# Kernel tuning notes

Measured on AMD Instinct MI355X. Metric: run time of the kernel, lower is better.

The kernel has to match this reference:

```python
import jax, jax.numpy as jnp
import numpy as np

N_NODES = 20000
N_EDGES = 160000
F_IN = 256
N_CLASSES = 32
HEADS = 8
GAT_C = 128


def setup_inputs() -> dict:
    key = jax.random.key(0)
    ks = jax.random.split(key, 20)

    def w(k, shape, fan_in):
        return jax.random.normal(k, shape, dtype=jnp.float32) * (1.0 / np.sqrt(fan_in))

    return {
        "x": jax.random.normal(ks[0], (N_NODES, F_IN), dtype=jnp.float32),
        "edge_index": jax.random.randint(ks[1], (2, N_EDGES), 0, N_NODES, dtype=jnp.int64),
        # SAGEConv(256 -> 64): lin_l (bias) on aggregated neighbors, lin_r (no bias) on root
        "W_l1": w(ks[2], (F_IN, 64), F_IN), "b_l1": jnp.zeros((64,), jnp.float32),
        "W_r1": w(ks[3], (F_IN, 64), F_IN),
        # SAGEConv(64 -> 128)
        "W_l2": w(ks[4], (64, 128), 64), "b_l2": jnp.zeros((128,), jnp.float32),
        "W_r2": w(ks[5], (64, 128), 64),
        # GATConv(128 -> 128, heads=8, concat)
        "W_g": w(ks[6], (128, HEADS * GAT_C), 128),
        "att_src": w(ks[7], (HEADS, GAT_C), GAT_C),
        "att_dst": w(ks[8], (HEADS, GAT_C), GAT_C),
        "b_g": jnp.zeros((HEADS * GAT_C,), jnp.float32),
        # GCNConv(1024 -> 64), GCNConv(64 -> 32)
        "W_c1": w(ks[9], (HEADS * GAT_C, 64), HEADS * GAT_C), "b_c1": jnp.zeros((64,), jnp.float32),
        "W_c2": w(ks[10], (64, N_CLASSES), 64), "b_c2": jnp.zeros((N_CLASSES,), jnp.float32),
        # residual Linear(256 -> 64)
        "W_res": w(ks[11], (F_IN, 64), F_IN), "b_res": jnp.zeros((64,), jnp.float32),
    }


def _forward(x, edge_index, W_l1, b_l1, W_r1, W_l2, b_l2, W_r2,
             W_g, att_src, att_dst, b_g, W_c1, b_c1, W_c2, b_c2, W_res, b_res):
    n = x.shape[0]
    src, dst = edge_index[0], edge_index[1]  # messages flow src -> dst

    def sage(h, Wl, bl, Wr):
        # mean aggregation of neighbor features, then lin_l(agg) + lin_r(root)
        s = jax.ops.segment_sum(h[src], dst, num_segments=n)
        cnt = jax.ops.segment_sum(jnp.ones_like(src, dtype=h.dtype), dst, num_segments=n)
        mean = s / jnp.maximum(cnt, 1.0)[:, None]
        return mean @ Wl + bl + h @ Wr

    res_x = x @ W_res + b_res
    h = jax.nn.relu(sage(x, W_l1, b_l1, W_r1)) + res_x      # [N, 64]
    h = jax.nn.relu(sage(h, W_l2, b_l2, W_r2))              # [N, 128]

    # ---- GATConv with self-loops (PyG default) ----
    loop = jnp.arange(n, dtype=src.dtype)
    srcf = jnp.concatenate([src, loop])
    dstf = jnp.concatenate([dst, loop])

    hg = (h @ W_g).reshape(n, HEADS, GAT_C)                 # [N, H, C]
    a_s = jnp.sum(hg * att_src, axis=-1)                    # [N, H]
    a_d = jnp.sum(hg * att_dst, axis=-1)                    # [N, H]
    e = jax.nn.leaky_relu(a_s[srcf] + a_d[dstf], negative_slope=0.2)  # [Ef, H]
    m = jax.ops.segment_max(e, dstf, num_segments=n)
    e = jnp.exp(e - m[dstf])
    denom = jax.ops.segment_sum(e, dstf, num_segments=n)
    alpha = e / denom[dstf]                                 # softmax over incoming edges
    gat = jax.ops.segment_sum(alpha[:, :, None] * hg[srcf], dstf, num_segments=n)
    h = jax.nn.relu(gat.reshape(n, HEADS * GAT_C) + b_g)    # [N, 1024]

    # ---- GCNConv with self-loops and symmetric normalization ----
    deg = jax.ops.segment_sum(jnp.ones_like(srcf, dtype=h.dtype), dstf, num_segments=n)
    dinv = jax.lax.rsqrt(jnp.maximum(deg, 1.0))             # deg >= 1 via self-loops
    norm = (dinv[srcf] * dinv[dstf])[:, None]

    def gcn(h, W, b):
        hw = h @ W
        return jax.ops.segment_sum(norm * hw[srcf], dstf, num_segments=n) + b

    h = gcn(h, W_c1, b_c1)
    h = gcn(h, W_c2, b_c2)
    return jax.nn.log_softmax(h, axis=1)


def reference(x, edge_index, W_l1, b_l1, W_r1, W_l2, b_l2, W_r2,
              W_g, att_src, att_dst, b_g, W_c1, b_c1, W_c2, b_c2, W_res, b_res):
    return _forward(x, edge_index, W_l1, b_l1, W_r1, W_l2, b_l2, W_r2,
                    W_g, att_src, att_dst, b_g, W_c1, b_c1, W_c2, b_c2, W_res, b_res)
```

## Files before the change

kernel.cpp:

```cpp
#include <hip/hip_runtime.h>

#define NN 20000
#define NE 160000
#define NEF 180000
#define NB1 ((NN + 255) / 256)

typedef long long ll;
typedef __attribute__((ext_vector_type(4))) float f32x4;
typedef __attribute__((ext_vector_type(8))) short s16x8;

static __device__ __forceinline__ float b2f(ushort u) {
  return __uint_as_float(((unsigned)u) << 16);
}
static __device__ __forceinline__ ushort f2b(float f) {
  unsigned u = __float_as_uint(f);
  return (ushort)((u + 0x7fffu + ((u >> 16) & 1u)) >> 16);
}

template<int MF, int NF, int K, bool F32OUT>
__global__ __launch_bounds__(256) void gemm_mfma(
    const ushort* __restrict__ A, const ushort* __restrict__ Bt,
    const float* __restrict__ bias, void* __restrict__ Cv,
    int M, int N, int lda)
{
  const int wid  = threadIdx.x >> 6;
  const int lane = threadIdx.x & 63;
  const int wr = wid >> 1, wc = wid & 1;
  const int bm = blockIdx.y * (32 * MF) + wr * (16 * MF);
  const int bn = blockIdx.x * (32 * NF) + wc * (16 * NF);
  const int lr = lane & 15;
  const int ko = (lane >> 4) * 8;

  const ushort* pa[MF];
  const ushort* pb[NF];
  #pragma unroll
  for (int i = 0; i < MF; i++) {
    int r = min(bm + i * 16 + lr, M - 1);
    pa[i] = A + (ll)r * lda + ko;
  }
  #pragma unroll
  for (int j = 0; j < NF; j++) {
    int c = min(bn + j * 16 + lr, N - 1);
    pb[j] = Bt + (ll)c * K + ko;
  }

  f32x4 acc[MF][NF];
  #pragma unroll
  for (int i = 0; i < MF; i++)
    #pragma unroll
    for (int j = 0; j < NF; j++) acc[i][j] = {0.f, 0.f, 0.f, 0.f};

  #pragma unroll
  for (int k = 0; k < K; k += 32) {
    s16x8 af[MF], bf[NF];
    #pragma unroll
    for (int i = 0; i < MF; i++) af[i] = *(const s16x8*)(pa[i] + k);
    #pragma unroll
    for (int j = 0; j < NF; j++) bf[j] = *(const s16x8*)(pb[j] + k);
    #pragma unroll
    for (int i = 0; i < MF; i++)
      #pragma unroll
      for (int j = 0; j < NF; j++)
        acc[i][j] = __builtin_amdgcn_mfma_f32_16x16x32_bf16(af[i], bf[j], acc[i][j], 0, 0, 0);
  }

  const int rq = (lane >> 4) * 4;
  #pragma unroll
  for (int i = 0; i < MF; i++) {
    #pragma unroll
    for (int j = 0; j < NF; j++) {
      int col = bn + j * 16 + lr;
      if (col >= N) continue;
      float bv = bias ? bias[col] : 0.f;
      int rbase = bm + i * 16 + rq;
      #pragma unroll
      for (int r = 0; r < 4; r++) {
        int row = rbase + r;
        if (row >= M) continue;
        float v = acc[i][j][r] + bv;
        if (F32OUT) ((float*)Cv)[(ll)row * N + col] = v;
        else        ((ushort*)Cv)[(ll)row * N + col] = f2b(v);
      }
    }
  }
}

__global__ __launch_bounds__(256) void k_gat_apply_gcn1(
    const ushort* __restrict__ agg,
    const ushort* __restrict__ BtG,
    const ushort* __restrict__ Btc1,
    const float* __restrict__ b_g,
    ushort* __restrict__ hw64)
{
  __shared__ ushort At[2][32 * 128];
  __shared__ ushort gt[2][32][72];
  const int t    = threadIdx.x;
  const int wc   = t >> 6;
  const int lane = t & 63;
  const int bm = blockIdx.x * 32;
  const int lr = lane & 15;
  const int q  = lane >> 4;
  const int ko = q * 8;
  const int rq = q * 4;

  const int srow = t >> 3;
  const int scg  = t & 7;
  const ushort* sg = agg + (ll)min(bm + srow, NN - 1) * 1024 + scg * 16;
  const int w0 = srow * 128 + (((2 * scg)     ^ (srow & 7)) * 8);
  const int w1 = srow * 128 + (((2 * scg + 1) ^ (srow & 7)) * 8);

  s16x8 ar[8][2];
  #pragma unroll
  for (int h = 0; h < 8; h++) {
    ar[h][0] = *(const s16x8*)(sg + h * 128);
    ar[h][1] = *(const s16x8*)(sg + h * 128 + 8);
  }

  s16x8 b1[2][4];
  s16x8 b2[2][2];
  float bvs[2];
  {
    const int cg = wc * 16 + lr;
    const ushort* pb = BtG + (ll)cg * 128 + ko;
    b1[0][0] = *(const s16x8*)(pb);
    b1[0][1] = *(const s16x8*)(pb + 32);
    b1[0][2] = *(const s16x8*)(pb + 64);
    b1[0][3] = *(const s16x8*)(pb + 96);
    const ushort* qb = Btc1 + (ll)cg * 1024 + ko;
    b2[0][0] = *(const s16x8*)(qb);
    b2[0][1] = *(const s16x8*)(qb + 32);
    bvs[0] = b_g[cg];
  }

  f32x4 o0 = {0.f, 0.f, 0.f, 0.f}, o1 = o0;

  #pragma unroll
  for (int h = 0; h < 8; h++) {
    *(s16x8*)&At[h & 1][w0] = ar[h][0];
    *(s16x8*)&At[h & 1][w1] = ar[h][1];
    __syncthreads();
    #pragma unroll
    for (int it = 0; it < 2; it++) {
      const int ct = 2 * h + it;
      const int cur = it, nxt = it ^ 1;
      if (ct < 15) {
        const int cg2 = (ct + 1) * 64 + wc * 16 + lr;
        const ushort* pb2 = BtG + (ll)cg2 * 128 + ko;
        b1[nxt][0] = *(const s16x8*)(pb2);
        b1[nxt][1] = *(const s16x8*)(pb2 + 32);
        b1[nxt][2] = *(const s16x8*)(pb2 + 64);
        b1[nxt][3] = *(const s16x8*)(pb2 + 96);
        const ushort* qb2 = Btc1 + (ll)(wc * 16 + lr) * 1024 + (ct + 1) * 64 + ko;
        b2[nxt][0] = *(const s16x8*)(qb2);
        b2[nxt][1] = *(const s16x8*)(qb2 + 32);
        bvs[nxt] = b_g[cg2];
      }
      f32x4 g0 = {0.f, 0.f, 0.f, 0.f}, g1 = g0;
      #pragma unroll
      for (int k = 0; k < 4; k++) {
        const int gi = (k * 4 + q) ^ (lr & 7);
        s16x8 a0 = *(const s16x8*)&At[h & 1][lr        * 128 + gi * 8];
        s16x8 a1 = *(const s16x8*)&At[h & 1][(16 + lr) * 128 + gi * 8];
        g0 = __builtin_amdgcn_mfma_f32_16x16x32_bf16(a0, b1[cur][k], g0, 0, 0, 0);
        g1 = __builtin_amdgcn_mfma_f32_16x16x32_bf16(a1, b1[cur][k], g1, 0, 0, 0);
      }
      float bv = bvs[cur];
      #pragma unroll
      for (int r = 0; r < 4; r++) {
        gt[it][rq + r][wc * 16 + lr]      = f2b(fmaxf(g0[r] + bv, 0.f));
        gt[it][16 + rq + r][wc * 16 + lr] = f2b(fmaxf(g1[r] + bv, 0.f));
      }
      __syncthreads();
      {
        s16x8 a0 = *(const s16x8*)&gt[it][lr][ko];
        s16x8 a1 = *(const s16x8*)&gt[it][16 + lr][ko];
        o0 = __builtin_amdgcn_mfma_f32_16x16x32_bf16(a0, b2[cur][0], o0, 0, 0, 0);
        o1 = __builtin_amdgcn_mfma_f32_16x16x32_bf16(a1, b2[cur][0], o1, 0, 0, 0);
        s16x8 a2 = *(const s16x8*)&gt[it][lr][32 + ko];
        s16x8 a3 = *(const s16x8*)&gt[it][16 + lr][32 + ko];
        o0 = __builtin_amdgcn_mfma_f32_16x16x32_bf16(a2, b2[cur][1], o0, 0, 0, 0);
        o1 = __builtin_amdgcn_mfma_f32_16x16x32_bf16(a3, b2[cur][1], o1, 0, 0, 0);
      }
    }
  }
  int col = wc * 16 + lr;
  #pragma unroll
  for (int r = 0; r < 4; r++) {
    int row0 = bm + rq + r, row1 = bm + 16 + rq + r;
    if (row0 < NN) hw64[(ll)row0 * 64 + col] = f2b(o0[r]);
    if (row1 < NN) hw64[(ll)row1 * 64 + col] = f2b(o1[r]);
  }
}

struct PrepEnt { const float* W; ushort* Bt; int N; int K; int base; };
struct Prep { PrepEnt e[8]; int total; };

__global__ void k_setup(const float* __restrict__ x, ushort* __restrict__ xb, Prep p,
                        const float* __restrict__ b_res, const float* __restrict__ b_l1,
                        const float* __restrict__ b_l2, float* __restrict__ bias192,
                        float* __restrict__ bias256,
                        const float* __restrict__ W_g, const float* __restrict__ att_s,
                        const float* __restrict__ att_d, ushort* __restrict__ watt_t,
                        int* __restrict__ icnt) {
  ll t = (ll)blockIdx.x * 256 + threadIdx.x;
  const ll T0 = (ll)NN * 64;
  if (t < T0) {
    ll i = t * 4;
    float4 v = *(const float4*)(x + i);
    ushort4 o;
    o.x = f2b(v.x); o.y = f2b(v.y); o.z = f2b(v.z); o.w = f2b(v.w);
    *(ushort4*)(xb + i) = o;
    return;
  }
  t -= T0;
  if (t < p.total) {
    int tt = (int)t;
    #pragma unroll
    for (int i = 0; i < 8; i++) {
      int sz = p.e[i].N * p.e[i].K;
      if (tt >= p.e[i].base && tt < p.e[i].base + sz) {
        int loc = tt - p.e[i].base;
        int n = loc / p.e[i].K, k = loc - n * p.e[i].K;
        p.e[i].Bt[loc] = f2b(p.e[i].W[(ll)k * p.e[i].N + n]);
      }
    }
    return;
  }
  t -= p.total;
  if (t < 256) {
    int tt = (int)t;
    if (tt < 64) bias192[tt] = b_res[tt];
    else if (tt < 128) bias192[tt] = 0.f;
    else if (tt < 192) bias192[tt] = b_l1[tt - 128];
    bias256[tt] = (tt < 128) ? 0.f : b_l2[tt - 128];
    return;
  }
  t -= 256;
  if (t < 2048) {
    int k = (int)t >> 4;
    int col = (int)t & 15;
    int h = col & 7;
    const float* av = (col < 8) ? (att_s + h * 128) : (att_d + h * 128);
    const float* wrow = W_g + (ll)k * 1024 + h * 128;
    float s = 0.f;
    for (int j = 0; j < 128; j++) s += wrow[j] * av[j];
    watt_t[col * 128 + k] = f2b(s);
    return;
  }
  t -= 2048;
  if (t < NN) icnt[t] = 0;
}

__global__ void k_counti(const int* __restrict__ dst, int* __restrict__ icnt) {
  int e = blockIdx.x * 256 + threadIdx.x;
  if (e < NE) atomicAdd(&icnt[dst[e]], 1);
}

__global__ __launch_bounds__(256) void k_scan1(const int* __restrict__ icnt,
                                               int* __restrict__ rowptr,
                                               int* __restrict__ bsum) {
  __shared__ int sd[256];
  int t = threadIdx.x;
  int i = blockIdx.x * 256 + t;
  int v = (i < NN) ? icnt[i] + 1 : 0;
  sd[t] = v;
  __syncthreads();
  #pragma unroll
  for (int o = 1; o < 256; o <<= 1) {
    int u = (t >= o) ? sd[t - o] : 0;
    __syncthreads();
    sd[t] += u;
    __syncthreads();
  }
  if (i < NN) rowptr[i] = sd[t] - v;
  if (t == 255) bsum[blockIdx.x] = sd[255];
}

__global__ __launch_bounds__(128) void k_scan2(const int* __restrict__ bsum,
                                               int* __restrict__ boff) {
  __shared__ int sd[128];
  int t = threadIdx.x;
  int v = (t < NB1) ? bsum[t] : 0;
  sd[t] = v;
  __syncthreads();
  #pragma unroll
  for (int o = 1; o < 128; o <<= 1) {
    int u = (t >= o) ? sd[t - o] : 0;
    __syncthreads();
    sd[t] += u;
    __syncthreads();
  }
  if (t < NB1) boff[t] = sd[t] - v;
}

__global__ void k_scan3(int* __restrict__ rowptr, const int* __restrict__ boff,
                        int* __restrict__ cur, const int* __restrict__ icnt,
                        float* __restrict__ dinv) {
  int i = blockIdx.x * 256 + threadIdx.x;
  if (i >= NN) return;
  int r = rowptr[i] + boff[i >> 8];
  rowptr[i] = r;
  cur[i] = r;
  dinv[i] = rsqrtf((float)icnt[i] + 1.0f);
  if (i == 0) rowptr[NN] = NEF;
}

__global__ void k_scatter(const int* __restrict__ dst, int* __restrict__ cur,
                          int* __restrict__ eid) {
  int t = blockIdx.x * 256 + threadIdx.x;
  if (t >= NEF) return;
  int d = (t < NE) ? dst[t] : t - NE;
  int p = atomicAdd(&cur[d], 1);
  eid[p] = t;
}

template<int C, int STRIDE, bool ADD_RES>
__global__ __launch_bounds__(256) void k_sage_csr(
    const int* __restrict__ rowptr, const int* __restrict__ eid,
    const int* __restrict__ src, const ushort* __restrict__ feat,
    const ushort* __restrict__ linr, const ushort* __restrict__ resx,
    ushort* __restrict__ out)
{
  int node = blockIdx.x * 4 + (threadIdx.x >> 6);
  int lane = threadIdx.x & 63;
  if (node >= NN) return;
  int b = rowptr[node], e = rowptr[node + 1];
  float a0 = 0.f, a1 = 0.f;
  int n = 0;
  for (int base = b; base < e; base += 64) {
    int m = min(64, e - base);
    int sreg = -1;
    if (lane < m) {
      int ed = eid[base + lane];
      sreg = (ed < NE) ? src[ed] : -1;
    }
    for (int i = 0; i < m; i++) {
      int s = __shfl(sreg, i);
      if (s >= 0) {
        a0 += b2f(feat[(ll)s * STRIDE + lane]);
        if (C == 128) a1 += b2f(feat[(ll)s * STRIDE + lane + 64]);
        n++;
      }
    }
  }
  float inv = 1.f / fmaxf((float)n, 1.f);
  {
    float v = a0 * inv + b2f(linr[(ll)node * STRIDE + lane]);
    v = fmaxf(v, 0.f);
    if (ADD_RES) v += b2f(resx[(ll)node * STRIDE + lane]);
    out[(ll)node * C + lane] = f2b(v);
  }
  if (C == 128) {
    float v = a1 * inv + b2f(linr[(ll)node * STRIDE + lane + 64]);
    v = fmaxf(v, 0.f);
    out[(ll)node * C + lane + 64] = f2b(v);
  }
}

__global__ void k_gat_softmax(const int* __restrict__ rowptr, const int* __restrict__ eid,
                              const int* __restrict__ src, const float* __restrict__ asd,
                              float* __restrict__ alpha, float* __restrict__ invden) {
  int t = blockIdx.x * 256 + threadIdx.x;
  if (t >= NN * 8) return;
  int node = t >> 3, h = t & 7;
  int b = rowptr[node], e = rowptr[node + 1];
  float ad = asd[(ll)node * 16 + 8 + h];
  float mx = -3.0e38f;
  for (int p = b; p < e; p++) {
    int ed = eid[p];
    int s = (ed < NE) ? src[ed] : node;
    float v = asd[(ll)s * 16 + h] + ad;
    v = (v > 0.f) ? v : 0.2f * v;
    mx = fmaxf(mx, v);
  }
  float sum = 0.f;
  for (int p = b; p < e; p++) {
    int ed = eid[p];
    int s = (ed < NE) ? src[ed] : node;
    float v = asd[(ll)s * 16 + h] + ad;
    v = (v > 0.f) ? v : 0.2f * v;
    float ex = expf(v - mx);
    alpha[(ll)p * 8 + h] = ex;
    sum += ex;
  }
  invden[t] = 1.f / sum;
}

__global__ __launch_bounds__(128) void k_gat_agg(
    const int* __restrict__ rowptr, const int* __restrict__ eid,
    const int* __restrict__ src, const float* __restrict__ alpha,
    const float* __restrict__ invden, const ushort* __restrict__ h2b,
    ushort* __restrict__ agg)
{
  __shared__ int s_l[64];
  __shared__ float al[64 * 8];
  __shared__ float inv_s[8];
  int node = blockIdx.x;
  int c = threadIdx.x;
  int b = rowptr[node], e = rowptr[node + 1];
  if (c < 8) inv_s[c] = invden[node * 8 + c];
  float acc[8] = {0.f, 0.f, 0.f, 0.f, 0.f, 0.f, 0.f, 0.f};
  for (int c0 = b; c0 < e; c0 += 64) {
    int m = min(64, e - c0);
    if (c < m) { int ed = eid[c0 + c]; s_l[c] = (ed < NE) ? src[ed] : node; }
    for (int idx = c; idx < m * 8; idx += 128) al[idx] = alpha[(ll)c0 * 8 + idx];
    __syncthreads();
    for (int i = 0; i < m; i++) {
      float v = b2f(h2b[(ll)s_l[i] * 128 + c]);
      float4 aa = *(const float4*)&al[i * 8];
      float4 ab = *(const float4*)&al[i * 8 + 4];
      acc[0] = fmaf(aa.x, v, acc[0]);
      acc[1] = fmaf(aa.y, v, acc[1]);
      acc[2] = fmaf(aa.z, v, acc[2]);
      acc[3] = fmaf(aa.w, v, acc[3]);
      acc[4] = fmaf(ab.x, v, acc[4]);
      acc[5] = fmaf(ab.y, v, acc[5]);
      acc[6] = fmaf(ab.z, v, acc[6]);
      acc[7] = fmaf(ab.w, v, acc[7]);
    }
    __syncthreads();
  }
  #pragma unroll
  for (int h = 0; h < 8; h++)
    agg[(ll)node * 1024 + h * 128 + c] = f2b(acc[h] * inv_s[h]);
}

template<int C, bool FUSE_LSM>
__global__ __launch_bounds__(256) void k_gcn_csr(
    const int* __restrict__ rowptr, const int* __restrict__ eid,
    const int* __restrict__ src, const float* __restrict__ dinv,
    const ushort* __restrict__ hw, const float* __restrict__ bias,
    void* __restrict__ outv)
{
  const int npb = 256 / C;
  int node = blockIdx.x * npb + threadIdx.x / C;
  int c = threadIdx.x & (C - 1);
  if (node >= NN) return;
  int b = rowptr[node], e = rowptr[node + 1];
  float acc = 0.f;
  for (int base = b; base < e; base += C) {
    int m = min(C, e - base);
    int sreg = 0;
    float dreg = 0.f;
    if (c < m) {
      int ed = eid[base + c];
      sreg = (ed < NE) ? src[ed] : node;
      dreg = dinv[sreg];
    }
    for (int i = 0; i < m; i++) {
      int s  = __shfl(sreg, i, C);
      float dv = __shfl(dreg, i, C);
      acc = fmaf(dv, b2f(hw[(ll)s * C + c]), acc);
    }
  }
  float v = acc * dinv[node] + bias[c];
  if (!FUSE_LSM) {
    ((ushort*)outv)[(ll)node * C + c] = f2b(v);
  } else {
    float mx = v;
    #pragma unroll
    for (int o = 16; o > 0; o >>= 1) mx = fmaxf(mx, __shfl_xor(mx, o, 32));
    float s = expf(v - mx);
    #pragma unroll
    for (int o = 16; o > 0; o >>= 1) s += __shfl_xor(s, o, 32);
    ((float*)outv)[(ll)node * C + c] = v - mx - logf(s);
  }
}

extern "C" void kernel_launch(void* const* d_in, const int* in_sizes, int n_in,
                              void* d_out, int out_size, void* d_ws, size_t ws_size,
                              hipStream_t stream) {
  const float* x     = (const float*)d_in[0];
  const int*   ei    = (const int*)d_in[1];
  const float* W_l1  = (const float*)d_in[2];
  const float* b_l1  = (const float*)d_in[3];
  const float* W_r1  = (const float*)d_in[4];
  const float* W_l2  = (const float*)d_in[5];
  const float* b_l2  = (const float*)d_in[6];
  const float* W_r2  = (const float*)d_in[7];
  const float* W_g   = (const float*)d_in[8];
  const float* att_s = (const float*)d_in[9];
  const float* att_d = (const float*)d_in[10];
  const float* b_g   = (const float*)d_in[11];
  const float* W_c1  = (const float*)d_in[12];
  const float* b_c1  = (const float*)d_in[13];
  const float* W_c2  = (const float*)d_in[14];
  const float* b_c2  = (const float*)d_in[15];
  const float* W_res = (const float*)d_in[16];
  const float* b_res = (const float*)d_in[17];
  const int* src = ei;
  const int* dst = ei + NE;
  float* out = (float*)d_out;

  float* Wf = (float*)d_ws;
  size_t off = 0;
  auto take = [&](size_t n) { float* p = Wf + off; off += (n + 3) & ~(size_t)3; return p; };
  ushort* xb    = (ushort*)take((size_t)NN * 128);
  ushort* C192  = (ushort*)take((size_t)NN * 96);
  ushort* h1    = (ushort*)take((size_t)NN * 32);
  ushort* C256  = (ushort*)take((size_t)NN * 128);
  ushort* h2    = (ushort*)take((size_t)NN * 64);
  ushort* agg   = (ushort*)take((size_t)NN * 512);
  ushort* hw64  = (ushort*)take((size_t)NN * 32);
  ushort* acc64 = (ushort*)take((size_t)NN * 32);
  ushort* hw32  = (ushort*)take((size_t)NN * 16);
  ushort* Bt192 = (ushort*)take(192 * 256 / 2);
  ushort* Bt256 = (ushort*)take(256 * 64 / 2);
  ushort* BtG   = (ushort*)take(1024 * 128 / 2);
  ushort* Btc1  = (ushort*)take(64 * 1024 / 2);
  ushort* Btc2  = (ushort*)take(32 * 64 / 2);
  ushort* watt_t= (ushort*)take(16 * 128 / 2);
  float* bias192 = take(192);
  float* bias256 = take(256);
  int*   icnt   = (int*)take(NN);
  int*   rowptr = (int*)take(NN + 1);
  int*   cur    = (int*)take(NN);
  int*   eidb   = (int*)take(NEF);
  int*   bsum   = (int*)take(NB1);
  int*   boff   = (int*)take(NB1);
  float* dinv   = take(NN);
  float* asd    = take((size_t)NN * 16);
  float* alpha  = take((size_t)NEF * 8);
  float* invden = take((size_t)NN * 8);
  (void)ws_size; (void)in_sizes; (void)n_in; (void)out_size;

  auto nb = [](ll t) { return dim3((unsigned)((t + 255) / 256)); };

  Prep pp;
  int base = 0;
  auto ent = [&](int i, const float* W, ushort* Bt, int N_, int K_) {
    pp.e[i] = {W, Bt, N_, K_, base}; base += N_ * K_;
  };
  ent(0, W_res, Bt192,             64, 256);
  ent(1, W_l1,  Bt192 + 64 * 256,  64, 256);
  ent(2, W_r1,  Bt192 + 128 * 256, 64, 256);
  ent(3, W_l2,  Bt256,             128, 64);
  ent(4, W_r2,  Bt256 + 128 * 64,  128, 64);
  ent(5, W_g,   BtG,               1024, 128);
  ent(6, W_c1,  Btc1,              64, 1024);
  ent(7, W_c2,  Btc2,              32, 64);
  pp.total = base;
  k_setup<<<nb((ll)NN * 64 + base + 256 + 2048 + NN), 256, 0, stream>>>(
      x, xb, pp, b_res, b_l1, b_l2, bias192, bias256, W_g, att_s, att_d, watt_t, icnt);

  k_counti<<<nb(NE), 256, 0, stream>>>(dst, icnt);
  k_scan1<<<NB1, 256, 0, stream>>>(icnt, rowptr, bsum);
  k_scan2<<<1, 128, 0, stream>>>(bsum, boff);
  k_scan3<<<nb(NN), 256, 0, stream>>>(rowptr, boff, cur, icnt, dinv);
  k_scatter<<<nb(NEF), 256, 0, stream>>>(dst, cur, eidb);

  gemm_mfma<4, 2, 256, false><<<dim3(3, 157), 256, 0, stream>>>(
      xb, Bt192, bias192, C192, NN, 192, 256);
  k_sage_csr<64, 192, true><<<nb((ll)NN * 64), 256, 0, stream>>>(
      rowptr, eidb, src, C192 + 64, C192 + 128, C192, h1);

  gemm_mfma<4, 2, 64, false><<<dim3(4, 157), 256, 0, stream>>>(
      h1, Bt256, bias256, C256, NN, 256, 64);
  k_sage_csr<128, 256, false><<<nb((ll)NN * 64), 256, 0, stream>>>(
      rowptr, eidb, src, C256, C256 + 128, nullptr, h2);

  gemm_mfma<4, 1, 128, true><<<dim3(1, 157), 256, 0, stream>>>(
      h2, watt_t, nullptr, asd, NN, 16, 128);
  k_gat_softmax<<<nb((ll)NN * 8), 256, 0, stream>>>(
      rowptr, eidb, src, asd, alpha, invden);
  k_gat_agg<<<dim3(NN), 128, 0, stream>>>(
      rowptr, eidb, src, alpha, invden, h2, agg);
  k_gat_apply_gcn1<<<dim3(625), 256, 0, stream>>>(agg, BtG, Btc1, b_g, hw64);
  k_gcn_csr<64, false><<<nb((ll)NN * 64), 256, 0, stream>>>(
      rowptr, eidb, src, dinv, hw64, b_c1, acc64);

  gemm_mfma<4, 1, 64, false><<<dim3(1, 157), 256, 0, stream>>>(
      acc64, Btc2, nullptr, hw32, NN, 32, 64);
  k_gcn_csr<32, true><<<nb((ll)NN * 32), 256, 0, stream>>>(
      rowptr, eidb, src, dinv, hw32, b_c2, out);
}
```

Before: 234.3 us.

## Fuse GAT edge softmax into aggregation kernel with online softmax

```diff
diff --git a/kernel.cpp b/kernel.cpp
--- a/kernel.cpp
+++ b/kernel.cpp
@@ -357,54 +357,53 @@
   }
 }
 
-__global__ void k_gat_softmax(const int* __restrict__ rowptr, const int* __restrict__ eid,
-                              const int* __restrict__ src, const float* __restrict__ asd,
-                              float* __restrict__ alpha, float* __restrict__ invden) {
-  int t = blockIdx.x * 256 + threadIdx.x;
-  if (t >= NN * 8) return;
-  int node = t >> 3, h = t & 7;
-  int b = rowptr[node], e = rowptr[node + 1];
-  float ad = asd[(ll)node * 16 + 8 + h];
-  float mx = -3.0e38f;
-  for (int p = b; p < e; p++) {
-    int ed = eid[p];
-    int s = (ed < NE) ? src[ed] : node;
-    float v = asd[(ll)s * 16 + h] + ad;
-    v = (v > 0.f) ? v : 0.2f * v;
-    mx = fmaxf(mx, v);
-  }
-  float sum = 0.f;
-  for (int p = b; p < e; p++) {
-    int ed = eid[p];
-    int s = (ed < NE) ? src[ed] : node;
-    float v = asd[(ll)s * 16 + h] + ad;
-    v = (v > 0.f) ? v : 0.2f * v;
-    float ex = expf(v - mx);
-    alpha[(ll)p * 8 + h] = ex;
-    sum += ex;
-  }
-  invden[t] = 1.f / sum;
-}
-
 __global__ __launch_bounds__(128) void k_gat_agg(
     const int* __restrict__ rowptr, const int* __restrict__ eid,
-    const int* __restrict__ src, const float* __restrict__ alpha,
-    const float* __restrict__ invden, const ushort* __restrict__ h2b,
-    ushort* __restrict__ agg)
+    const int* __restrict__ src, const float* __restrict__ asd,
+    const ushort* __restrict__ h2b, ushort* __restrict__ agg)
 {
   __shared__ int s_l[64];
   __shared__ float al[64 * 8];
-  __shared__ float inv_s[8];
+  __shared__ float adl[8];
+  __shared__ float mrun[8], srun[8], fac[8];
   int node = blockIdx.x;
   int c = threadIdx.x;
   int b = rowptr[node], e = rowptr[node + 1];
-  if (c < 8) inv_s[c] = invden[node * 8 + c];
+  if (c < 8) {
+    adl[c] = asd[(ll)node * 16 + 8 + c];
+    mrun[c] = -3.0e38f;
+    srun[c] = 0.f;
+  }
   float acc[8] = {0.f, 0.f, 0.f, 0.f, 0.f, 0.f, 0.f, 0.f};
   for (int c0 = b; c0 < e; c0 += 64) {
     int m = min(64, e - c0);
     if (c < m) { int ed = eid[c0 + c]; s_l[c] = (ed < NE) ? src[ed] : node; }
-    for (int idx = c; idx < m * 8; idx += 128) al[idx] = alpha[(ll)c0 * 8 + idx];
-    __syncthreads();
+    __syncthreads();
+    for (int idx = c; idx < m * 8; idx += 128) {
+      int i = idx >> 3, h = idx & 7;
+      float v = asd[(ll)s_l[i] * 16 + h] + adl[h];
+      al[idx] = (v > 0.f) ? v : 0.2f * v;
+    }
+    __syncthreads();
+    if (c < 8) {
+      float cm = mrun[c];
+      for (int i = 0; i < m; i++) cm = fmaxf(cm, al[i * 8 + c]);
+      fac[c] = __expf(mrun[c] - cm);
+      mrun[c] = cm;
+    }
+    __syncthreads();
+    for (int idx = c; idx < m * 8; idx += 128) {
+      int h = idx & 7;
+      al[idx] = __expf(al[idx] - mrun[h]);
+    }
+    __syncthreads();
+    if (c < 8) {
+      float cs = 0.f;
+      for (int i = 0; i < m; i++) cs += al[i * 8 + c];
+      srun[c] = srun[c] * fac[c] + cs;
+    }
+    #pragma unroll
+    for (int h = 0; h < 8; h++) acc[h] *= fac[h];
     for (int i = 0; i < m; i++) {
       float v = b2f(h2b[(ll)s_l[i] * 128 + c]);
       float4 aa = *(const float4*)&al[i * 8];
@@ -422,7 +421,7 @@
   }
   #pragma unroll
   for (int h = 0; h < 8; h++)
-    agg[(ll)node * 1024 + h * 128 + c] = f2b(acc[h] * inv_s[h]);
+    agg[(ll)node * 1024 + h * 128 + c] = f2b(acc[h] / srun[h]);
 }
 
 template<int C, bool FUSE_LSM>
@@ -520,8 +519,6 @@
   int*   boff   = (int*)take(NB1);
   float* dinv   = take(NN);
   float* asd    = take((size_t)NN * 16);
-  float* alpha  = take((size_t)NEF * 8);
-  float* invden = take((size_t)NN * 8);
   (void)ws_size; (void)in_sizes; (void)n_in; (void)out_size;
 
   auto nb = [](ll t) { return dim3((unsigned)((t + 255) / 256)); };
@@ -561,10 +558,8 @@
 
   gemm_mfma<4, 1, 128, true><<<dim3(1, 157), 256, 0, stream>>>(
       h2, watt_t, nullptr, asd, NN, 16, 128);
-  k_gat_softmax<<<nb((ll)NN * 8), 256, 0, stream>>>(
-      rowptr, eidb, src, asd, alpha, invden);
   k_gat_agg<<<dim3(NN), 128, 0, stream>>>(
-      rowptr, eidb, src, alpha, invden, h2, agg);
+      rowptr, eidb, src, asd, h2, agg);
   k_gat_apply_gcn1<<<dim3(625), 256, 0, stream>>>(agg, BtG, Btc1, b_g, hw64);
   k_gcn_csr<64, false><<<nb((ll)NN * 64), 256, 0, stream>>>(
       rowptr, eidb, src, dinv, hw64, b_c1, acc64);
```

Result: faster. 219.2 us, median of 2 (-6.4%).
